# Optimization experiments

Hardware: AMD Instinct MI355X
Metric: run time of the kernel (lower is better)

Reference implementation:

```python
import jax, jax.numpy as jnp
import numpy as np

N_NODES = 40000
N_EDGES = 640000
IN_FEATS = 256
EDGE_FEATS = 64
OUT_FEATS = 128
NUM_HEADS = 8
D = OUT_FEATS // NUM_HEADS  # 16


def setup_inputs() -> dict:
    key = jax.random.key(0)
    ks = jax.random.split(key, 9)
    node_feats = jax.random.normal(ks[0], (N_NODES, IN_FEATS), dtype=jnp.float32)
    edge_feats = jax.random.normal(ks[1], (N_EDGES, EDGE_FEATS), dtype=jnp.float32)
    src = jax.random.randint(ks[2], (N_EDGES,), 0, N_NODES, dtype=jnp.int32)
    dst = jax.random.randint(ks[3], (N_EDGES,), 0, N_NODES, dtype=jnp.int32)
    # learned parameters (xavier-ish scale)
    node_w = jax.random.normal(ks[4], (OUT_FEATS, IN_FEATS), dtype=jnp.float32) * (2.0 / (IN_FEATS + OUT_FEATS)) ** 0.5
    node_b = jnp.zeros((OUT_FEATS,), dtype=jnp.float32)
    edge_w = jax.random.normal(ks[5], (OUT_FEATS, EDGE_FEATS), dtype=jnp.float32) * (2.0 / (EDGE_FEATS + OUT_FEATS)) ** 0.5
    edge_b = jnp.zeros((OUT_FEATS,), dtype=jnp.float32)
    attn = jax.random.normal(ks[6], (1, NUM_HEADS, 3 * D), dtype=jnp.float32) * 0.1
    return {"node_feats": node_feats, "edge_feats": edge_feats, "src": src, "dst": dst,
            "node_w": node_w, "node_b": node_b, "edge_w": edge_w, "edge_b": edge_b, "attn": attn}


def reference(node_feats, edge_feats, src, dst, node_w, node_b, edge_w, edge_b, attn):
    N = node_feats.shape[0]
    # Node / edge projections -> [N,H,D], [E,H,D]
    Wh = (node_feats @ node_w.T + node_b).reshape(-1, NUM_HEADS, D)
    We = (edge_feats @ edge_w.T + edge_b).reshape(-1, NUM_HEADS, D)
    # Split attn into src/dst/edge parts: attn is [1,H,3D]
    a = attn[0]  # [H,3D]
    a_src, a_dst, a_e = a[:, :D], a[:, D:2 * D], a[:, 2 * D:]
    # Per-node partial scores [N,H], then gather per edge; edge part [E,H]
    s_src = jnp.einsum('nhd,hd->nh', Wh, a_src)
    s_dst = jnp.einsum('nhd,hd->nh', Wh, a_dst)
    s_e = jnp.einsum('ehd,hd->eh', We, a_e)
    e = s_src[src] + s_dst[dst] + s_e  # [E,H]
    e = jax.nn.leaky_relu(e, negative_slope=0.2)
    # Edge softmax over incoming edges of each dst node
    m = jax.ops.segment_max(e, dst, num_segments=N)          # [N,H]
    ex = jnp.exp(e - m[dst])                                  # [E,H]
    z = jax.ops.segment_sum(ex, dst, num_segments=N)          # [N,H]
    alpha = ex / z[dst]                                       # [E,H]
    # Weighted scatter-sum aggregation of source features
    msg = alpha[:, :, None] * Wh[src]                         # [E,H,D]
    h = jax.ops.segment_sum(msg, dst, num_segments=N)         # [N,H,D]
    return h.reshape(N, NUM_HEADS * D)
```

## Files before the change

### kernel.cpp

```cpp
#include <hip/hip_runtime.h>
#include <hip/hip_fp16.h>
#include <stdint.h>
#include <stddef.h>

#define N_NODES   40000
#define N_EDGES   640000
#define IN_FEATS  256
#define EDGE_FEATS 64
#define OUT_FEATS 128
#define NUM_HEADS 8
#define HD        16

typedef __attribute__((ext_vector_type(8))) short  short8;
typedef __attribute__((ext_vector_type(4))) float  floatx4;

__device__ inline short f2bf(float f) {
  union { float f; uint32_t u; } v; v.f = f;
  uint32_t r = v.u + 0x7fffu + ((v.u >> 16) & 1u);
  return (short)(r >> 16);
}

__device__ inline short8 cvt8(float4 lo, float4 hi) {
  short8 r;
  r[0] = f2bf(lo.x); r[1] = f2bf(lo.y); r[2] = f2bf(lo.z); r[3] = f2bf(lo.w);
  r[4] = f2bf(hi.x); r[5] = f2bf(hi.y); r[6] = f2bf(hi.z); r[7] = f2bf(hi.w);
  return r;
}

__device__ inline float bflo(uint32_t w) {
  union { uint32_t u; float f; } v; v.u = w << 16; return v.f;
}
__device__ inline float bfhi(uint32_t w) {
  union { uint32_t u; float f; } v; v.u = w & 0xffff0000u; return v.f;
}

__global__ __launch_bounds__(512) void prep_hist_kernel(
    const float* __restrict__ edge_w, const float* __restrict__ edge_b,
    const float* __restrict__ attn, const float* __restrict__ node_w,
    const int* __restrict__ dst,
    float* __restrict__ Wfold, float* __restrict__ bfold,
    uint32_t* __restrict__ Wbf, int* __restrict__ deg) {
  int tid = threadIdx.x;
  if (blockIdx.x == 0) {
    int h = tid >> 6, k = tid & 63;
    float s = 0.f;
    #pragma unroll
    for (int d = 0; d < HD; d++)
      s += edge_w[(h * HD + d) * EDGE_FEATS + k] * attn[h * 48 + 32 + d];
    Wfold[h * EDGE_FEATS + k] = s;
    if (k == 0) {
      float b = 0.f;
      #pragma unroll
      for (int d = 0; d < HD; d++)
        b += edge_b[h * HD + d] * attn[h * 48 + 32 + d];
      bfold[h] = b;
    }
    const float2* W2 = (const float2*)node_w;
    #pragma unroll
    for (int j = 0; j < 32; j++) {
      int p = j * 512 + tid;
      float2 f = W2[p];
      Wbf[p] = (uint32_t)(uint16_t)f2bf(f.x) |
               ((uint32_t)(uint16_t)f2bf(f.y) << 16);
    }
  } else {
    int e = (blockIdx.x - 1) * 512 + tid;
    atomicAdd(&deg[dst[e]], 1);
  }
}

__global__ __launch_bounds__(256) void wh_gemm(
    const float* __restrict__ A,
    const uint32_t* __restrict__ Wbf,
    const float* __restrict__ bias,
    uint32_t* __restrict__ Whp) {
  int wave = (blockIdx.x * blockDim.x + threadIdx.x) >> 6;
  int lane = threadIdx.x & 63;
  int m0 = wave * 16;
  if (m0 >= N_NODES) return;
  int row = lane & 15, quad = lane >> 4;

  floatx4 acc[8];
  #pragma unroll
  for (int nt = 0; nt < 8; nt++) acc[nt] = (floatx4)(0.f);

  const float4* A4 = (const float4*)A;
  const uint4*  W4 = (const uint4*)Wbf;
  int a_base = ((m0 + row) * IN_FEATS + quad * 8) >> 2;

  #pragma unroll
  for (int s = 0; s < 8; s++) {
    float4 alo = A4[a_base + s * 8];
    float4 ahi = A4[a_base + s * 8 + 1];
    short8 af = cvt8(alo, ahi);
    #pragma unroll
    for (int nt = 0; nt < 8; nt++) {
      int fo = (nt * 16 + row) * IN_FEATS + s * 32 + quad * 8;
      uint4 u = W4[fo >> 3];
      short8 bf = *(short8*)&u;
      acc[nt] = __builtin_amdgcn_mfma_f32_16x16x32_bf16(af, bf, acc[nt], 0, 0, 0);
    }
  }
  #pragma unroll
  for (int nt = 0; nt < 4; nt++) {
    float blo_ = bias[nt * 16 + row];
    float bhi_ = bias[64 + nt * 16 + row];
    #pragma unroll
    for (int r = 0; r < 4; r++) {
      int m = m0 + quad * 4 + r;
      float lo = acc[nt][r] + blo_;
      float hi = acc[nt + 4][r] + bhi_;
      uint32_t d = (uint32_t)(uint16_t)f2bf(lo) |
                   ((uint32_t)(uint16_t)f2bf(hi) << 16);
      Whp[m * 64 + nt * 16 + row] = d;
    }
  }
}

__global__ __launch_bounds__(256) void ssd_kernel(
    const uint32_t* __restrict__ Whp, const float* __restrict__ attn,
    float* __restrict__ s_src, float* __restrict__ s_dst) {
  int t = blockIdx.x * 256 + threadIdx.x;
  int n = t >> 2, hp = t & 3;
  const uint4* p = (const uint4*)(Whp + n * 64 + hp * 16);
  const float* as_lo = attn + hp * 48;
  const float* ad_lo = attn + hp * 48 + 16;
  const float* as_hi = attn + (hp + 4) * 48;
  const float* ad_hi = attn + (hp + 4) * 48 + 16;
  float ss_lo = 0.f, sd_lo = 0.f, ss_hi = 0.f, sd_hi = 0.f;
  #pragma unroll
  for (int q = 0; q < 4; q++) {
    uint4 u = p[q];
    uint32_t ws[4] = {u.x, u.y, u.z, u.w};
    #pragma unroll
    for (int k = 0; k < 4; k++) {
      int d = q * 4 + k;
      float lo = bflo(ws[k]), hi = bfhi(ws[k]);
      ss_lo += lo * as_lo[d]; sd_lo += lo * ad_lo[d];
      ss_hi += hi * as_hi[d]; sd_hi += hi * ad_hi[d];
    }
  }
  s_src[n * 8 + hp]     = ss_lo;
  s_src[n * 8 + hp + 4] = ss_hi;
  s_dst[n * 8 + hp]     = sd_lo;
  s_dst[n * 8 + hp + 4] = sd_hi;
}

__global__ __launch_bounds__(1024) void scan_kernel(
    const int* __restrict__ deg, int* __restrict__ rs, int* __restrict__ cursor) {
  __shared__ int wsum[40][16];
  int tid = threadIdx.x;
  int lane = tid & 63, w = tid >> 6;

  int ex[40];
  #pragma unroll
  for (int c = 0; c < 40; c++) {
    int i = c * 1024 + tid;
    int vv = (i < N_NODES) ? deg[i] : 0;
    int xv = vv;
    #pragma unroll
    for (int off = 1; off < 64; off <<= 1) {
      int y = __shfl_up(xv, off, 64);
      if (lane >= off) xv += y;
    }
    ex[c] = xv - vv;
    if (lane == 63) wsum[c][w] = xv;
  }
  __syncthreads();

  int carry = 0;
  #pragma unroll
  for (int c = 0; c < 40; c++) {
    int p = carry;
    #pragma unroll
    for (int j = 0; j < 16; j++) {
      int s = wsum[c][j];
      if (j < w) p += s;
      carry += s;
    }
    int i = c * 1024 + tid;
    if (i < N_NODES) {
      int excl = p + ex[c];
      rs[i] = excl;
      cursor[i] = excl;
    }
  }
  if (tid == 0) rs[N_NODES] = carry;
}

__global__ __launch_bounds__(256) void edge_scatter_kernel(
    const float* __restrict__ edge_feats, const int* __restrict__ src,
    const int* __restrict__ dst, const float* __restrict__ Wfold,
    const float* __restrict__ bfold, const float* __restrict__ s_src,
    const float* __restrict__ s_dst, int* __restrict__ cursor,
    uint32_t* __restrict__ rec) {
  __shared__ float4 efs[16 * 256];
  int tid = threadIdx.x;
  int e0 = blockIdx.x * 256;
  int e = e0 + tid;
  int s = src[e], d = dst[e];
  int pos = atomicAdd(&cursor[d], 1);

  const float4* ss4 = (const float4*)(s_src + (size_t)s * 8);
  const float4* sd4 = (const float4*)(s_dst + (size_t)d * 8);
  float4 sa = ss4[0], sb = ss4[1];
  float4 da = sd4[0], db = sd4[1];

  const float4* base = (const float4*)(edge_feats + (size_t)e0 * EDGE_FEATS);
  #pragma unroll
  for (int j = 0; j < 16; j++) {
    int p = j * 256 + tid;
    float4 v = base[p];
    int k4 = p & 15;
    int edge = p >> 4;
    efs[k4 * 256 + (edge ^ (k4 & 7))] = v;
  }
  __syncthreads();

  float acc[8];
  #pragma unroll
  for (int h = 0; h < 8; h++) acc[h] = bfold[h];
  #pragma unroll
  for (int k4 = 0; k4 < 16; k4++) {
    float4 f = efs[k4 * 256 + (tid ^ (k4 & 7))];
    #pragma unroll
    for (int h = 0; h < 8; h++) {
      const float* wr = Wfold + h * EDGE_FEATS + k4 * 4;
      acc[h] += f.x * wr[0] + f.y * wr[1] + f.z * wr[2] + f.w * wr[3];
    }
  }
  float v[8];
  v[0] = acc[0] + sa.x + da.x; v[1] = acc[1] + sa.y + da.y;
  v[2] = acc[2] + sa.z + da.z; v[3] = acc[3] + sa.w + da.w;
  v[4] = acc[4] + sb.x + db.x; v[5] = acc[5] + sb.y + db.y;
  v[6] = acc[6] + sb.z + db.z; v[7] = acc[7] + sb.w + db.w;
  #pragma unroll
  for (int h = 0; h < 8; h++) v[h] = v[h] > 0.f ? v[h] : 0.2f * v[h];

  uint32_t pk[4];
  #pragma unroll
  for (int j = 0; j < 4; j++) {
    uint32_t lo = __half_as_ushort(__float2half_rn(v[2 * j]));
    uint32_t hi = __half_as_ushort(__float2half_rn(v[2 * j + 1]));
    pk[j] = lo | (hi << 16);
  }
  uint32_t* r = rec + (size_t)pos * 8;
  *(uint4*)r = make_uint4(pk[0], pk[1], pk[2], pk[3]);
  r[4] = (uint32_t)s;
}

__global__ __launch_bounds__(256) void aggregate_kernel(
    const int* __restrict__ rs, const uint32_t* __restrict__ rec,
    const uint32_t* __restrict__ Whp, float* __restrict__ out) {
  int node = blockIdx.x * 4 + (threadIdx.x >> 6);
  int lane = threadIdx.x & 63;
  int h1 = lane >> 4;
  int start = rs[node], end = rs[node + 1];
  uint32_t sh = (h1 & 1) * 16;
  bool hi_pair = (h1 & 2) != 0;

  float z1 = 0.f, z2 = 0.f, a1 = 0.f, a2 = 0.f;

  #define STEP(g, wv)                                                  \
    {                                                                  \
      uint32_t c1 = hi_pair ? (g).y : (g).x;                           \
      uint32_t c2 = hi_pair ? (g).w : (g).z;                           \
      float l1 = __half2float(__ushort_as_half((uint16_t)(c1 >> sh))); \
      float l2 = __half2float(__ushort_as_half((uint16_t)(c2 >> sh))); \
      float e1 = __expf(l1), e2 = __expf(l2);                          \
      z1 += e1; z2 += e2;                                              \
      a1 += e1 * bflo(wv); a2 += e2 * bfhi(wv);                        \
    }

  int i = start;
  for (; i + 3 < end; i += 4) {
    const uint32_t* r0 = rec + (size_t)i * 8;
    uint4 g0 = *(const uint4*)(r0);
    uint4 g1 = *(const uint4*)(r0 + 8);
    uint4 g2 = *(const uint4*)(r0 + 16);
    uint4 g3 = *(const uint4*)(r0 + 24);
    int s0 = (int)r0[4], s1 = (int)r0[12], s2 = (int)r0[20], s3 = (int)r0[28];
    uint32_t w0 = Whp[(size_t)s0 * 64 + lane];
    uint32_t w1 = Whp[(size_t)s1 * 64 + lane];
    uint32_t w2 = Whp[(size_t)s2 * 64 + lane];
    uint32_t w3 = Whp[(size_t)s3 * 64 + lane];
    STEP(g0, w0); STEP(g1, w1); STEP(g2, w2); STEP(g3, w3);
  }
  for (; i < end; i++) {
    const uint32_t* r0 = rec + (size_t)i * 8;
    uint4 g0 = *(const uint4*)(r0);
    int s0 = (int)r0[4];
    uint32_t w0 = Whp[(size_t)s0 * 64 + lane];
    STEP(g0, w0);
  }
  #undef STEP

  float o1 = (end > start) ? a1 / z1 : 0.f;
  float o2 = (end > start) ? a2 / z2 : 0.f;
  out[(size_t)node * OUT_FEATS + lane] = o1;
  out[(size_t)node * OUT_FEATS + 64 + lane] = o2;
}

extern "C" void kernel_launch(void* const* d_in, const int* in_sizes, int n_in,
                              void* d_out, int out_size, void* d_ws, size_t ws_size,
                              hipStream_t stream) {
  const float* node_feats = (const float*)d_in[0];
  const float* edge_feats = (const float*)d_in[1];
  const int*   src        = (const int*)d_in[2];
  const int*   dst        = (const int*)d_in[3];
  const float* node_w     = (const float*)d_in[4];
  const float* node_b     = (const float*)d_in[5];
  const float* edge_w     = (const float*)d_in[6];
  const float* edge_b     = (const float*)d_in[7];
  const float* attn       = (const float*)d_in[8];
  float* out = (float*)d_out;

  char* ws = (char*)d_ws;
  size_t off = 0;
  auto alloc = [&](size_t bytes) {
    void* p = ws + off;
    off += (bytes + 255) & ~(size_t)255;
    return p;
  };
  uint32_t* Whp      = (uint32_t*)alloc((size_t)N_NODES * 64 * 4);
  float*    s_src    = (float*)alloc((size_t)N_NODES * NUM_HEADS * 4);
  float*    s_dst    = (float*)alloc((size_t)N_NODES * NUM_HEADS * 4);
  uint32_t* rec      = (uint32_t*)alloc((size_t)N_EDGES * 32);
  int*      deg      = (int*)alloc((size_t)N_NODES * 4);
  int*      rs       = (int*)alloc((size_t)(N_NODES + 1) * 4);
  int*      cursor   = (int*)alloc((size_t)N_NODES * 4);
  float*    Wfold    = (float*)alloc(NUM_HEADS * EDGE_FEATS * 4);
  float*    bfold    = (float*)alloc(NUM_HEADS * 4);
  uint32_t* Wbf      = (uint32_t*)alloc((size_t)OUT_FEATS * IN_FEATS * 2);

  hipMemsetAsync(deg, 0, (size_t)N_NODES * 4, stream);

  prep_hist_kernel<<<1 + N_EDGES / 512, 512, 0, stream>>>(
      edge_w, edge_b, attn, node_w, dst, Wfold, bfold, Wbf, deg);
  wh_gemm<<<N_NODES / 16 / 4, 256, 0, stream>>>(node_feats, Wbf, node_b, Whp);
  ssd_kernel<<<N_NODES * 4 / 256, 256, 0, stream>>>(Whp, attn, s_src, s_dst);
  scan_kernel<<<1, 1024, 0, stream>>>(deg, rs, cursor);
  edge_scatter_kernel<<<N_EDGES / 256, 256, 0, stream>>>(
      edge_feats, src, dst, Wfold, bfold, s_src, s_dst, cursor, rec);
  aggregate_kernel<<<N_NODES / 4, 256, 0, stream>>>(rs, rec, Whp, out);
}
```

Measured before the change: 409.1 us.

## Fuse projection GEMM, score reduction, histogram and weight fold into one kernel

Three launches (prep/histogram, node GEMM, per-node score kernel) are merged into one heterogeneous kernel whose blocks split into GEMM, degree-histogram and fold roles. The GEMM now converts node_w to bf16 on the fly and computes s_src/s_dst from fp32 accumulators with wave shuffles, so there is no longer a separate pass that re-reads Whp. The edge scatter kernel stages edge features through shared memory in two halves, halving LDS use to raise occupancy at the cost of an extra barrier. Side effect: the scores are now computed from unrounded values, and the on-the-fly conversion repeats the weight cast in every wave.

```diff
diff --git a/kernel.cpp b/kernel.cpp
--- a/kernel.cpp
+++ b/kernel.cpp
@@ -11,6 +11,10 @@
 #define NUM_HEADS 8
 #define HD        16
 
+#define WH_BLOCKS   625
+#define HIST_BLOCKS 2500
+#define FOLD_BLOCK  (WH_BLOCKS + HIST_BLOCKS)
+
 typedef __attribute__((ext_vector_type(8))) short  short8;
 typedef __attribute__((ext_vector_type(4))) float  floatx4;
 
@@ -34,116 +38,111 @@
   union { uint32_t u; float f; } v; v.u = w & 0xffff0000u; return v.f;
 }
 
-__global__ __launch_bounds__(512) void prep_hist_kernel(
+__global__ __launch_bounds__(256) void fused_head_kernel(
+    const float* __restrict__ A,
+    const float* __restrict__ node_w,
+    const float* __restrict__ bias,
     const float* __restrict__ edge_w, const float* __restrict__ edge_b,
-    const float* __restrict__ attn, const float* __restrict__ node_w,
-    const int* __restrict__ dst,
+    const float* __restrict__ attn, const int* __restrict__ dst,
+    int* __restrict__ deg,
     float* __restrict__ Wfold, float* __restrict__ bfold,
-    uint32_t* __restrict__ Wbf, int* __restrict__ deg) {
+    uint32_t* __restrict__ Whp,
+    float* __restrict__ s_src, float* __restrict__ s_dst) {
+  int bid = blockIdx.x;
   int tid = threadIdx.x;
-  if (blockIdx.x == 0) {
-    int h = tid >> 6, k = tid & 63;
-    float s = 0.f;
-    #pragma unroll
-    for (int d = 0; d < HD; d++)
-      s += edge_w[(h * HD + d) * EDGE_FEATS + k] * attn[h * 48 + 32 + d];
-    Wfold[h * EDGE_FEATS + k] = s;
-    if (k == 0) {
+
+  if (bid < WH_BLOCKS) {
+    int wave = (bid * 256 + tid) >> 6;
+    int lane = tid & 63;
+    int m0 = wave * 16;
+    int row = lane & 15, quad = lane >> 4;
+
+    floatx4 acc[8];
+    #pragma unroll
+    for (int nt = 0; nt < 8; nt++) acc[nt] = (floatx4)(0.f);
+
+    const float4* A4  = (const float4*)A;
+    const float4* Wf4 = (const float4*)node_w;
+    int a_base = ((m0 + row) * IN_FEATS + quad * 8) >> 2;
+
+    #pragma unroll
+    for (int s = 0; s < 8; s++) {
+      float4 alo = A4[a_base + s * 8];
+      float4 ahi = A4[a_base + s * 8 + 1];
+      short8 af = cvt8(alo, ahi);
+      #pragma unroll
+      for (int nt = 0; nt < 8; nt++) {
+        int fo = (nt * 16 + row) * IN_FEATS + s * 32 + quad * 8;
+        float4 blo = Wf4[fo >> 2];
+        float4 bhi = Wf4[(fo >> 2) + 1];
+        short8 bf = cvt8(blo, bhi);
+        acc[nt] = __builtin_amdgcn_mfma_f32_16x16x32_bf16(af, bf, acc[nt], 0, 0, 0);
+      }
+    }
+
+    float as_lo[4], ad_lo[4], as_hi[4], ad_hi[4];
+    #pragma unroll
+    for (int nt = 0; nt < 4; nt++) {
+      as_lo[nt] = attn[nt * 48 + row];
+      ad_lo[nt] = attn[nt * 48 + 16 + row];
+      as_hi[nt] = attn[(nt + 4) * 48 + row];
+      ad_hi[nt] = attn[(nt + 4) * 48 + 16 + row];
+    }
+
+    #pragma unroll
+    for (int nt = 0; nt < 4; nt++) {
+      float blo_ = bias[nt * 16 + row];
+      float bhi_ = bias[64 + nt * 16 + row];
+      #pragma unroll
+      for (int r = 0; r < 4; r++) {
+        int m = m0 + quad * 4 + r;
+        float lo = acc[nt][r] + blo_;
+        float hi = acc[nt + 4][r] + bhi_;
+        uint32_t dpk = (uint32_t)(uint16_t)f2bf(lo) |
+                       ((uint32_t)(uint16_t)f2bf(hi) << 16);
+        Whp[m * 64 + nt * 16 + row] = dpk;
+
+        float v0 = lo * as_lo[nt];
+        float v1 = lo * ad_lo[nt];
+        float v2 = hi * as_hi[nt];
+        float v3 = hi * ad_hi[nt];
+        #pragma unroll
+        for (int mk = 1; mk < 16; mk <<= 1) {
+          v0 += __shfl_xor(v0, mk, 64);
+          v1 += __shfl_xor(v1, mk, 64);
+          v2 += __shfl_xor(v2, mk, 64);
+          v3 += __shfl_xor(v3, mk, 64);
+        }
+        if (row == nt * 4 + r) {
+          s_src[m * 8 + nt]     = v0;
+          s_dst[m * 8 + nt]     = v1;
+          s_src[m * 8 + nt + 4] = v2;
+          s_dst[m * 8 + nt + 4] = v3;
+        }
+      }
+    }
+  } else if (bid < FOLD_BLOCK) {
+    int e = (bid - WH_BLOCKS) * 256 + tid;
+    atomicAdd(&deg[dst[e]], 1);
+  } else {
+    #pragma unroll
+    for (int it = 0; it < 2; it++) {
+      int idx = it * 256 + tid;
+      int h = idx >> 6, k = idx & 63;
+      float s = 0.f;
+      #pragma unroll
+      for (int d = 0; d < HD; d++)
+        s += edge_w[(h * HD + d) * EDGE_FEATS + k] * attn[h * 48 + 32 + d];
+      Wfold[h * EDGE_FEATS + k] = s;
+    }
+    if (tid < 8) {
       float b = 0.f;
       #pragma unroll
       for (int d = 0; d < HD; d++)
-        b += edge_b[h * HD + d] * attn[h * 48 + 32 + d];
-      bfold[h] = b;
-    }
-    const float2* W2 = (const float2*)node_w;
-    #pragma unroll
-    for (int j = 0; j < 32; j++) {
-      int p = j * 512 + tid;
-      float2 f = W2[p];
-      Wbf[p] = (uint32_t)(uint16_t)f2bf(f.x) |
-               ((uint32_t)(uint16_t)f2bf(f.y) << 16);
-    }
-  } else {
-    int e = (blockIdx.x - 1) * 512 + tid;
-    atomicAdd(&deg[dst[e]], 1);
-  }
-}
-
-__global__ __launch_bounds__(256) void wh_gemm(
-    const float* __restrict__ A,
-    const uint32_t* __restrict__ Wbf,
-    const float* __restrict__ bias,
-    uint32_t* __restrict__ Whp) {
-  int wave = (blockIdx.x * blockDim.x + threadIdx.x) >> 6;
-  int lane = threadIdx.x & 63;
-  int m0 = wave * 16;
-  if (m0 >= N_NODES) return;
-  int row = lane & 15, quad = lane >> 4;
-
-  floatx4 acc[8];
-  #pragma unroll
-  for (int nt = 0; nt < 8; nt++) acc[nt] = (floatx4)(0.f);
-
-  const float4* A4 = (const float4*)A;
-  const uint4*  W4 = (const uint4*)Wbf;
-  int a_base = ((m0 + row) * IN_FEATS + quad * 8) >> 2;
-
-  #pragma unroll
-  for (int s = 0; s < 8; s++) {
-    float4 alo = A4[a_base + s * 8];
-    float4 ahi = A4[a_base + s * 8 + 1];
-    short8 af = cvt8(alo, ahi);
-    #pragma unroll
-    for (int nt = 0; nt < 8; nt++) {
-      int fo = (nt * 16 + row) * IN_FEATS + s * 32 + quad * 8;
-      uint4 u = W4[fo >> 3];
-      short8 bf = *(short8*)&u;
-      acc[nt] = __builtin_amdgcn_mfma_f32_16x16x32_bf16(af, bf, acc[nt], 0, 0, 0);
-    }
-  }
-  #pragma unroll
-  for (int nt = 0; nt < 4; nt++) {
-    float blo_ = bias[nt * 16 + row];
-    float bhi_ = bias[64 + nt * 16 + row];
-    #pragma unroll
-    for (int r = 0; r < 4; r++) {
-      int m = m0 + quad * 4 + r;
-      float lo = acc[nt][r] + blo_;
-      float hi = acc[nt + 4][r] + bhi_;
-      uint32_t d = (uint32_t)(uint16_t)f2bf(lo) |
-                   ((uint32_t)(uint16_t)f2bf(hi) << 16);
-      Whp[m * 64 + nt * 16 + row] = d;
-    }
-  }
-}
-
-__global__ __launch_bounds__(256) void ssd_kernel(
-    const uint32_t* __restrict__ Whp, const float* __restrict__ attn,
-    float* __restrict__ s_src, float* __restrict__ s_dst) {
-  int t = blockIdx.x * 256 + threadIdx.x;
-  int n = t >> 2, hp = t & 3;
-  const uint4* p = (const uint4*)(Whp + n * 64 + hp * 16);
-  const float* as_lo = attn + hp * 48;
-  const float* ad_lo = attn + hp * 48 + 16;
-  const float* as_hi = attn + (hp + 4) * 48;
-  const float* ad_hi = attn + (hp + 4) * 48 + 16;
-  float ss_lo = 0.f, sd_lo = 0.f, ss_hi = 0.f, sd_hi = 0.f;
-  #pragma unroll
-  for (int q = 0; q < 4; q++) {
-    uint4 u = p[q];
-    uint32_t ws[4] = {u.x, u.y, u.z, u.w};
-    #pragma unroll
-    for (int k = 0; k < 4; k++) {
-      int d = q * 4 + k;
-      float lo = bflo(ws[k]), hi = bfhi(ws[k]);
-      ss_lo += lo * as_lo[d]; sd_lo += lo * ad_lo[d];
-      ss_hi += hi * as_hi[d]; sd_hi += hi * ad_hi[d];
-    }
-  }
-  s_src[n * 8 + hp]     = ss_lo;
-  s_src[n * 8 + hp + 4] = ss_hi;
-  s_dst[n * 8 + hp]     = sd_lo;
-  s_dst[n * 8 + hp + 4] = sd_hi;
+        b += edge_b[tid * HD + d] * attn[tid * 48 + 32 + d];
+      bfold[tid] = b;
+    }
+  }
 }
 
 __global__ __launch_bounds__(1024) void scan_kernel(
@@ -194,7 +193,7 @@
     const float* __restrict__ bfold, const float* __restrict__ s_src,
     const float* __restrict__ s_dst, int* __restrict__ cursor,
     uint32_t* __restrict__ rec) {
-  __shared__ float4 efs[16 * 256];
+  __shared__ float4 efs[8 * 256];
   int tid = threadIdx.x;
   int e0 = blockIdx.x * 256;
   int e = e0 + tid;
@@ -206,29 +205,34 @@
   float4 sa = ss4[0], sb = ss4[1];
   float4 da = sd4[0], db = sd4[1];
 
+  float acc[8];
+  #pragma unroll
+  for (int h = 0; h < 8; h++) acc[h] = bfold[h];
+
   const float4* base = (const float4*)(edge_feats + (size_t)e0 * EDGE_FEATS);
   #pragma unroll
-  for (int j = 0; j < 16; j++) {
-    int p = j * 256 + tid;
-    float4 v = base[p];
-    int k4 = p & 15;
-    int edge = p >> 4;
-    efs[k4 * 256 + (edge ^ (k4 & 7))] = v;
-  }
-  __syncthreads();
-
-  float acc[8];
-  #pragma unroll
-  for (int h = 0; h < 8; h++) acc[h] = bfold[h];
-  #pragma unroll
-  for (int k4 = 0; k4 < 16; k4++) {
-    float4 f = efs[k4 * 256 + (tid ^ (k4 & 7))];
-    #pragma unroll
-    for (int h = 0; h < 8; h++) {
-      const float* wr = Wfold + h * EDGE_FEATS + k4 * 4;
-      acc[h] += f.x * wr[0] + f.y * wr[1] + f.z * wr[2] + f.w * wr[3];
-    }
-  }
+  for (int P = 0; P < 2; P++) {
+    if (P) __syncthreads();
+    #pragma unroll
+    for (int j = 0; j < 8; j++) {
+      int q = j * 256 + tid;
+      int edge = q >> 3, kk = q & 7;
+      float4 v = base[edge * 16 + P * 8 + kk];
+      efs[kk * 256 + (edge ^ kk)] = v;
+    }
+    __syncthreads();
+    #pragma unroll
+    for (int kk = 0; kk < 8; kk++) {
+      float4 f = efs[kk * 256 + (tid ^ kk)];
+      int k4 = P * 8 + kk;
+      #pragma unroll
+      for (int h = 0; h < 8; h++) {
+        const float* wr = Wfold + h * EDGE_FEATS + k4 * 4;
+        acc[h] += f.x * wr[0] + f.y * wr[1] + f.z * wr[2] + f.w * wr[3];
+      }
+    }
+  }
+
   float v[8];
   v[0] = acc[0] + sa.x + da.x; v[1] = acc[1] + sa.y + da.y;
   v[2] = acc[2] + sa.z + da.z; v[3] = acc[3] + sa.w + da.w;
@@ -331,14 +335,12 @@
   int*      cursor   = (int*)alloc((size_t)N_NODES * 4);
   float*    Wfold    = (float*)alloc(NUM_HEADS * EDGE_FEATS * 4);
   float*    bfold    = (float*)alloc(NUM_HEADS * 4);
-  uint32_t* Wbf      = (uint32_t*)alloc((size_t)OUT_FEATS * IN_FEATS * 2);
 
   hipMemsetAsync(deg, 0, (size_t)N_NODES * 4, stream);
 
-  prep_hist_kernel<<<1 + N_EDGES / 512, 512, 0, stream>>>(
-      edge_w, edge_b, attn, node_w, dst, Wfold, bfold, Wbf, deg);
-  wh_gemm<<<N_NODES / 16 / 4, 256, 0, stream>>>(node_feats, Wbf, node_b, Whp);
-  ssd_kernel<<<N_NODES * 4 / 256, 256, 0, stream>>>(Whp, attn, s_src, s_dst);
+  fused_head_kernel<<<WH_BLOCKS + HIST_BLOCKS + 1, 256, 0, stream>>>(
+      node_feats, node_w, node_b, edge_w, edge_b, attn, dst, deg,
+      Wfold, bfold, Whp, s_src, s_dst);
   scan_kernel<<<1, 1024, 0, stream>>>(deg, rs, cursor);
   edge_scatter_kernel<<<N_EDGES / 256, 256, 0, stream>>>(
       edge_feats, src, dst, Wfold, bfold, s_src, s_dst, cursor, rec);
```

Measured after the change: 430.3 us. 5.2% more time.
